# Performance work log

Measured on AMD Instinct MI355X. Metric: run time of the kernel, lower is better.

The kernel has to match this reference:

```python
import jax, jax.numpy as jnp
import numpy as np

COMMITMENT_BETA = 0.25


def setup_inputs() -> dict:
    key = jax.random.key(0)
    k1, k2 = jax.random.split(key)
    B, D, H, W = 32, 256, 32, 32
    NUM_CODES = 1024
    z = jax.random.normal(k1, (B, D, H, W), dtype=jnp.float32)
    codebook = jax.random.normal(k2, (NUM_CODES, D), dtype=jnp.float32)
    return {"z": z, "codebook": codebook}


def reference(z, codebook):
    # z: [B, D, H, W], codebook: [K, D]
    B, D, H, W = z.shape
    z_flat = jnp.transpose(z, (0, 2, 3, 1)).reshape(-1, D)  # [N, D]
    # squared euclidean distances: ||z||^2 - 2 z.W^T + ||W||^2  -> [N, K]
    d = (
        jnp.sum(z_flat * z_flat, axis=1, keepdims=True)
        - 2.0 * (z_flat @ codebook.T)
        + jnp.sum(codebook * codebook, axis=1)[None, :]
    )
    indices = jnp.argmin(d, axis=1)  # [N]
    z_q_flat = codebook[indices]  # [N, D] gather
    # commitment loss: mse(z_flat, stop_grad(z_q_flat))
    diff = z_flat - jax.lax.stop_gradient(z_q_flat)
    commitment_loss = jnp.mean(diff * diff)
    # straight-through estimator
    z_q_flat = z_flat + jax.lax.stop_gradient(z_q_flat - z_flat)
    z_q = jnp.transpose(z_q_flat.reshape(B, H, W, D), (0, 3, 1, 2))
    indices = indices.reshape(B, H, W)
    return z_q, indices, COMMITMENT_BETA * commitment_loss
```

## Files before the change

### kernel.cpp

```cpp
#include <hip/hip_runtime.h>
#include <hip/hip_bf16.h>
#include <hip/hip_fp16.h>

#define DD  256
#define HWD 1024
#define NN  32768
#define KK  1024
#define ZQ_SIZE (NN*DD)
#define IDX_OFF ZQ_SIZE
#define LOSS_OFF (ZQ_SIZE + NN)

#define CBH_OFF    0
#define CNORM_OFF  (KK*DD*2)
#define ZSQ_OFF    (CNORM_OFF + KK*4)
#define ROWREC_OFF (ZSQ_OFF + 4096)

#define TH_REFINE 0.2f
#define LOSS_SCALE (0.25f / (float)ZQ_SIZE)

typedef __attribute__((ext_vector_type(8))) _Float16 h16x8;
typedef __attribute__((ext_vector_type(4))) float f32x4;

__device__ __forceinline__ void gload16(const void* g, void* l) {
    __builtin_amdgcn_global_load_lds(
        (const __attribute__((address_space(1))) void*)g,
        (__attribute__((address_space(3))) void*)l, 16, 0, 0);
}
__device__ __forceinline__ short f16bits(float x) {
    _Float16 h = (_Float16)x;
    return *reinterpret_cast<short*>(&h);
}
__device__ __forceinline__ void ins3(float v, float k, float& u1, float& e1,
                                     float& u2, float& e2, float& u3, float& e3) {
    bool l1 = v < u1, l2 = v < u2, l3 = v < u3;
    u3 = l2 ? u2 : (l3 ? v : u3);  e3 = l2 ? e2 : (l3 ? k : e3);
    u2 = l1 ? u1 : (l2 ? v : u2);  e2 = l1 ? e1 : (l2 ? k : e2);
    u1 = l1 ? v : u1;              e1 = l1 ? k : e1;
}

__global__ __launch_bounds__(256)
void vq_prep_kernel(const float* __restrict__ cb, unsigned char* __restrict__ scratch) {
    _Float16* cbh = (_Float16*)(scratch + CBH_OFF);
    float* cn = (float*)(scratch + CNORM_OFF);
    int t = threadIdx.x;
    int row = blockIdx.x * 16 + (t >> 4);
    int dq  = t & 15;
    const float* rp = cb + (size_t)row * DD + dq * 16;
    float nrm = 0.f;
    __attribute__((aligned(16))) _Float16 h[16];
#pragma unroll
    for (int i = 0; i < 4; ++i) {
        float4 v = *(const float4*)(rp + i * 4);
        float xs[4] = {v.x, v.y, v.z, v.w};
#pragma unroll
        for (int j = 0; j < 4; ++j) {
            float x = xs[j];
            h[i * 4 + j] = (_Float16)x;
            nrm = fmaf(x, x, nrm);
        }
    }
    *(uint4*)&cbh[(size_t)row * DD + dq * 16]     = *(uint4*)&h[0];
    *(uint4*)&cbh[(size_t)row * DD + dq * 16 + 8] = *(uint4*)&h[8];
#pragma unroll
    for (int m = 1; m < 16; m <<= 1) nrm += __shfl_xor(nrm, m, 64);
    if (dq == 0) cn[row] = nrm;
}

__global__ __launch_bounds__(256) __attribute__((amdgpu_waves_per_eu(3, 3)))
void vq_mfma_argmin_kernel(const float* __restrict__ z, unsigned char* __restrict__ scratch) {
    const unsigned char* cbh_b = scratch + CBH_OFF;
    const float* cn_g = (const float*)(scratch + CNORM_OFF);
    float* zsqp = (float*)(scratch + ZSQ_OFF);
    float* rowrec = (float*)(scratch + ROWREC_OFF);

    __shared__ __attribute__((aligned(16))) short bufs[3 * 8192];
    __shared__ float cn_l[512];
    __shared__ float zred[4];
    __shared__ float2 ep[2][64][3];

    const int t    = threadIdx.x;
    const int w    = t >> 6;
    const int lane = t & 63;
    const int ln15 = lane & 15;
    const int lh   = lane >> 4;
    const int g    = w >> 1;
    const int kq   = w & 1;

    const int bid = blockIdx.x;
    const int kh  = bid & 1;
    const int rt  = bid >> 1;
    const int n0  = rt * 64;
    const int b   = n0 >> 10;
    const int hw0 = n0 & 1023;

    const int ksub  = lane >> 5;
    const int chunk = lane & 31;

    const int klr   = kq * 16 + ln15;
    const int rbase = klr * 256;
    const int rxor  = (klr & 7) << 3;

    {
        float2 c = *(const float2*)(cn_g + kh * 512 + t * 2);
        *(float2*)&cn_l[t * 2] = c;
    }

    {
        short* zlds = bufs;
        const int zd = t >> 4;
        const int zq = t & 15;
        const float* zb = z + (size_t)b * DD * HWD + hw0 + zq * 4;
        float zsq = 0.f;
#pragma unroll
        for (int p = 0; p < 16; ++p) {
            int d = p * 16 + zd;
            float4 v = *(const float4*)(zb + (size_t)d * HWD);
            zsq = fmaf(v.x, v.x, zsq); zsq = fmaf(v.y, v.y, zsq);
            zsq = fmaf(v.z, v.z, zsq); zsq = fmaf(v.w, v.w, zsq);
            float xs[4] = {v.x, v.y, v.z, v.w};
#pragma unroll
            for (int i = 0; i < 4; ++i) {
                int row = zq * 4 + i;
                zlds[row * 256 + (d ^ ((row & 15) << 3))] = f16bits(xs[i]);
            }
        }
#pragma unroll
        for (int m = 1; m < 64; m <<= 1) zsq += __shfl_xor(zsq, m, 64);
        if (lane == 0) zred[w] = zsq;
    }
    __syncthreads();

    h16x8 ah[2][8];
#pragma unroll
    for (int nf = 0; nf < 2; ++nf)
#pragma unroll
        for (int ds = 0; ds < 8; ++ds) {
            int row = g * 32 + nf * 16 + ln15;
            int d0  = ds * 32 + lh * 8;
            ah[nf][ds] = *(const h16x8*)&bufs[row * 256 + (d0 ^ ((row & 15) << 3))];
        }
    if (kh == 0 && t == 0) zsqp[rt] = (zred[0] + zred[1]) + (zred[2] + zred[3]);
    __syncthreads();

    auto STAGE = [&](int tt) {
        short* dstb = &bufs[(tt % 3) * 8192];
#pragma unroll
        for (int si = 0; si < 4; ++si) {
            int s  = w * 4 + si;
            int kl = s * 2 + ksub;
            const unsigned char* src = cbh_b
                + (size_t)(kh * 512 + tt * 32 + kl) * 512 + ((chunk ^ (kl & 7)) << 4);
            gload16(src, &dstb[s * 512]);
        }
    };

    float v1[8], k1f[8], v2[8], k2f[8];
#pragma unroll
    for (int s = 0; s < 8; ++s) { v1[s] = 3e38f; v2[s] = 3e38f; k1f[s] = 0.f; k2f[s] = 0.f; }

    auto COMPUTE = [&](int kt) {
        const short* cbt = &bufs[(kt % 3) * 8192];
        const float cnv = cn_l[kt * 32 + klr];
        const float kgf = (float)(kh * 512 + kt * 32 + klr);
        f32x4 c0 = {0.f,0.f,0.f,0.f}, c1 = c0, c2 = c0, c3 = c0;
#pragma unroll
        for (int ds = 0; ds < 8; ds += 2) {
            const int ib0 = rbase + (((ds + 0) * 32 + lh * 8) ^ rxor);
            const int ib1 = rbase + (((ds + 1) * 32 + lh * 8) ^ rxor);
            h16x8 b0 = *(const h16x8*)&cbt[ib0];
            h16x8 b1 = *(const h16x8*)&cbt[ib1];
            c0 = __builtin_amdgcn_mfma_f32_16x16x32_f16(ah[0][ds + 0], b0, c0, 0, 0, 0);
            c2 = __builtin_amdgcn_mfma_f32_16x16x32_f16(ah[1][ds + 0], b0, c2, 0, 0, 0);
            c1 = __builtin_amdgcn_mfma_f32_16x16x32_f16(ah[0][ds + 1], b1, c1, 0, 0, 0);
            c3 = __builtin_amdgcn_mfma_f32_16x16x32_f16(ah[1][ds + 1], b1, c3, 0, 0, 0);
        }
        f32x4 s0 = c0 + c1, s1 = c2 + c3;
#pragma unroll
        for (int s = 0; s < 8; ++s) {
            float a = (s < 4) ? s0[s] : s1[s - 4];
            float dist = fmaf(-2.f, a, cnv);
            bool b1c = dist < v1[s];
            bool b2c = dist < v2[s];
            v2[s]  = b1c ? v1[s]  : (b2c ? dist : v2[s]);
            k2f[s] = b1c ? k1f[s] : (b2c ? kgf  : k2f[s]);
            v1[s]  = b1c ? dist : v1[s];
            k1f[s] = b1c ? kgf  : k1f[s];
        }
    };

    STAGE(0); STAGE(1);

    for (int kt = 0; kt < 14; ++kt) {
        asm volatile("s_waitcnt vmcnt(4)" ::: "memory");
        __builtin_amdgcn_sched_barrier(0);
        __builtin_amdgcn_s_barrier();
        __builtin_amdgcn_sched_barrier(0);
        STAGE(kt + 2);
        COMPUTE(kt);
    }
    asm volatile("s_waitcnt vmcnt(4)" ::: "memory");
    __builtin_amdgcn_sched_barrier(0);
    __builtin_amdgcn_s_barrier();
    __builtin_amdgcn_sched_barrier(0);
    COMPUTE(14);
    asm volatile("s_waitcnt vmcnt(0)" ::: "memory");
    __builtin_amdgcn_sched_barrier(0);
    __builtin_amdgcn_s_barrier();
    __builtin_amdgcn_sched_barrier(0);
    COMPUTE(15);

    float u3[8], e3[8];
#pragma unroll
    for (int s = 0; s < 8; ++s) { u3[s] = 3e38f; e3[s] = 0.f; }
#pragma unroll
    for (int m = 1; m < 16; m <<= 1) {
#pragma unroll
        for (int s = 0; s < 8; ++s) {
            float o1 = __shfl_xor(v1[s],  m, 64);
            float p1 = __shfl_xor(k1f[s], m, 64);
            float o2 = __shfl_xor(v2[s],  m, 64);
            float p2 = __shfl_xor(k2f[s], m, 64);
            float o3 = __shfl_xor(u3[s],  m, 64);
            float p3 = __shfl_xor(e3[s],  m, 64);
            ins3(o1, p1, v1[s], k1f[s], v2[s], k2f[s], u3[s], e3[s]);
            ins3(o2, p2, v1[s], k1f[s], v2[s], k2f[s], u3[s], e3[s]);
            ins3(o3, p3, v1[s], k1f[s], v2[s], k2f[s], u3[s], e3[s]);
        }
    }
    __syncthreads();
    if (ln15 == 0) {
#pragma unroll
        for (int s = 0; s < 8; ++s) {
            int nf = s >> 2, r = s & 3;
            int row = g * 32 + nf * 16 + lh * 4 + r;
            ep[kq][row][0] = make_float2(v1[s], k1f[s]);
            ep[kq][row][1] = make_float2(v2[s], k2f[s]);
            ep[kq][row][2] = make_float2(u3[s], e3[s]);
        }
    }
    __syncthreads();
    if (t < 64) {
        float a1 = 3e38f, b1 = 0.f, a2 = 3e38f, b2 = 0.f, a3 = 3e38f, b3 = 0.f;
#pragma unroll
        for (int q = 0; q < 2; ++q)
#pragma unroll
            for (int e = 0; e < 3; ++e) {
                float2 x = ep[q][t][e];
                ins3(x.x, x.y, a1, b1, a2, b2, a3, b3);
            }
        size_t base = ((size_t)kh * NN + n0 + t) * 8;
        float4 ra; ra.x = a1; ra.y = b1; ra.z = a2; ra.w = b2;
        float4 rb; rb.x = a3; rb.y = b3; rb.z = 0.f; rb.w = 0.f;
        *(float4*)&rowrec[base]     = ra;
        *(float4*)&rowrec[base + 4] = rb;
    }
}

__global__ __launch_bounds__(256)
void vq_refine_kernel(const float* __restrict__ z, const float* __restrict__ cb,
                      const unsigned char* __restrict__ scratch, float* __restrict__ idx_out,
                      float* __restrict__ lossp) {
    const float* rowrec = (const float*)(scratch + ROWREC_OFF);
    const float* cn_g = (const float*)(scratch + CNORM_OFF);
    const float* zsqp = (const float*)(scratch + ZSQ_OFF);
    int n = blockIdx.x * 256 + threadIdx.x;
    int lane = threadIdx.x & 63;

    float u1 = 3e38f, u2 = 3e38f, u3 = 3e38f, e1 = 0.f, e2 = 0.f, e3 = 0.f;
#pragma unroll
    for (int h = 0; h < 2; ++h) {
        size_t base = ((size_t)h * NN + n) * 8;
        float4 ra = *(const float4*)&rowrec[base];
        float4 rb = *(const float4*)&rowrec[base + 4];
        ins3(ra.x, ra.y, u1, e1, u2, e2, u3, e3);
        ins3(ra.z, ra.w, u1, e1, u2, e2, u3, e3);
        ins3(rb.x, rb.y, u1, e1, u2, e2, u3, e3);
    }

    bool flag = (u2 - u1) <= TH_REFINE;
    float lp = 0.f;
    if (!flag) { idx_out[n] = e1; lp = u1; }

    unsigned long long mask = __ballot(flag);
    while (mask) {
        int li = __ffsll(mask) - 1;
        mask &= mask - 1;
        int nn  = __shfl(n, li);
        int kk1 = (int)__shfl(e1, li);
        int kk2 = (int)__shfl(e2, li);
        int kk3 = (int)__shfl(e3, li);
        int bb = nn >> 10, hw = nn & 1023;
        const float* zp  = z  + (size_t)bb * DD * HWD + hw;
        const float* c1p = cb + (size_t)kk1 * DD;
        const float* c2p = cb + (size_t)kk2 * DD;
        const float* c3p = cb + (size_t)kk3 * DD;
        float s1 = 0.f, s2 = 0.f, s3 = 0.f;
#pragma unroll
        for (int j = 0; j < 4; ++j) {
            int d = lane + 64 * j;
            float zv = zp[(size_t)d * HWD];
            s1 = fmaf(zv, c1p[d], s1);
            s2 = fmaf(zv, c2p[d], s2);
            s3 = fmaf(zv, c3p[d], s3);
        }
#pragma unroll
        for (int m = 32; m >= 1; m >>= 1) {
            s1 += __shfl_xor(s1, m, 64);
            s2 += __shfl_xor(s2, m, 64);
            s3 += __shfl_xor(s3, m, 64);
        }
        float d1 = cn_g[kk1] - 2.f * s1;
        float d2 = cn_g[kk2] - 2.f * s2;
        float d3 = cn_g[kk3] - 2.f * s3;
        float dch = d1; int kch = kk1;
        if (d2 < dch || (d2 == dch && kk2 < kch)) { dch = d2; kch = kk2; }
        if (d3 < dch || (d3 == dch && kk3 < kch)) { dch = d3; kch = kk3; }
        if (lane == 0) { idx_out[nn] = (float)kch; lp += dch; }
    }

    if (blockIdx.x == 0) {
        const float2 zv = *(const float2*)&zsqp[threadIdx.x * 2];
        lp += zv.x + zv.y;
    }
#pragma unroll
    for (int m = 32; m >= 1; m >>= 1) lp += __shfl_xor(lp, m, 64);
    __shared__ float bl[4];
    if (lane == 0) bl[threadIdx.x >> 6] = lp;
    __syncthreads();
    if (threadIdx.x == 0)
        atomicAdd(lossp, (bl[0] + bl[1] + bl[2] + bl[3]) * LOSS_SCALE);
}

__global__ __launch_bounds__(256)
void vq_gather_kernel(const float* __restrict__ cb, float* __restrict__ out) {
    const float* idxf = out + IDX_OFF;
    __shared__ float crow[64][257];
    __shared__ int kidx[64];
    int t = threadIdx.x;
    int w = t >> 6, lane = t & 63;
    int n0 = blockIdx.x * 64;
    int b = n0 >> 10, hw0 = n0 & 1023;
    if (t < 64) kidx[t] = (int)idxf[n0 + t];
    __syncthreads();
    for (int i = 0; i < 16; ++i) {
        int r = w * 16 + i;
        int k = kidx[r];
        float4 v = *(const float4*)(cb + (size_t)k * DD + lane * 4);
        crow[r][lane * 4 + 0] = v.x; crow[r][lane * 4 + 1] = v.y;
        crow[r][lane * 4 + 2] = v.z; crow[r][lane * 4 + 3] = v.w;
    }
    __syncthreads();
    const int zph = t >> 6, hwl = t & 63;
#pragma unroll 4
    for (int dd = 0; dd < 64; ++dd) {
        int d = dd * 4 + zph;
        size_t o = (size_t)b * (DD * HWD) + (size_t)d * HWD + hw0 + hwl;
        out[o] = crow[hwl][d];
    }
}

extern "C" void kernel_launch(void* const* d_in, const int* in_sizes, int n_in,
                              void* d_out, int out_size, void* d_ws, size_t ws_size,
                              hipStream_t stream) {
    const float* z  = (const float*)d_in[0];
    const float* cb = (const float*)d_in[1];
    float* out = (float*)d_out;
    unsigned char* scratch = (unsigned char*)d_out;

    hipMemsetAsync((void*)(out + LOSS_OFF), 0, sizeof(float), stream);

    vq_prep_kernel<<<64, 256, 0, stream>>>(cb, scratch);
    vq_mfma_argmin_kernel<<<1024, 256, 0, stream>>>(z, scratch);
    vq_refine_kernel<<<128, 256, 0, stream>>>(z, cb, scratch, out + IDX_OFF, out + LOSS_OFF);
    vq_gather_kernel<<<512, 256, 0, stream>>>(cb, out);
}
```

Before: 82.80 us.

## Split z fp16 conversion into prep kernel and double rows per argmin block

Moves the z transpose, fp16 conversion and norm computation into a separate prep kernel that writes row-major fp16 z to scratch. The argmin kernel now handles 128 rows per block (four 16-row fragments per wave), so each codebook tile staged into LDS is reused across twice as many rows. The codebook pipeline also deepens from three to four buffers. The trade-offs are an extra launch and a scratch round-trip for z, more registers per wave (occupancy hint lowered to 2), and half as many argmin blocks.

```diff
diff --git a/kernel.cpp b/kernel.cpp
--- a/kernel.cpp
+++ b/kernel.cpp
@@ -14,6 +14,7 @@
 #define CNORM_OFF  (KK*DD*2)
 #define ZSQ_OFF    (CNORM_OFF + KK*4)
 #define ROWREC_OFF (ZSQ_OFF + 4096)
+#define Z16_OFF    (4*1024*1024)
 
 #define TH_REFINE 0.2f
 #define LOSS_SCALE (0.25f / (float)ZQ_SIZE)
@@ -66,118 +67,122 @@
     if (dq == 0) cn[row] = nrm;
 }
 
-__global__ __launch_bounds__(256) __attribute__((amdgpu_waves_per_eu(3, 3)))
-void vq_mfma_argmin_kernel(const float* __restrict__ z, unsigned char* __restrict__ scratch) {
+__global__ __launch_bounds__(256)
+void vq_prepz_kernel(const float* __restrict__ z, unsigned char* __restrict__ scratch) {
+    short* z16 = (short*)(scratch + Z16_OFF);
+    float* zsqp = (float*)(scratch + ZSQ_OFF);
+    __shared__ short zl[64 * 256];
+    __shared__ float zred[4];
+    const int t = threadIdx.x, w = t >> 6, lane = t & 63;
+    const int n0 = blockIdx.x * 64;
+    const int b = n0 >> 10, hw0 = n0 & 1023;
+    const int zd = t >> 4;
+    const int zq = t & 15;
+    const float* zb = z + (size_t)b * DD * HWD + hw0 + zq * 4;
+    float zsq = 0.f;
+#pragma unroll
+    for (int p = 0; p < 16; ++p) {
+        int d = p * 16 + zd;
+        float4 v = *(const float4*)(zb + (size_t)d * HWD);
+        zsq = fmaf(v.x, v.x, zsq); zsq = fmaf(v.y, v.y, zsq);
+        zsq = fmaf(v.z, v.z, zsq); zsq = fmaf(v.w, v.w, zsq);
+        float xs[4] = {v.x, v.y, v.z, v.w};
+#pragma unroll
+        for (int i = 0; i < 4; ++i) {
+            int row = zq * 4 + i;
+            zl[row * 256 + (d ^ ((row & 7) << 3))] = f16bits(xs[i]);
+        }
+    }
+#pragma unroll
+    for (int m = 1; m < 64; m <<= 1) zsq += __shfl_xor(zsq, m, 64);
+    if (lane == 0) zred[w] = zsq;
+    __syncthreads();
+    if (t == 0) zsqp[blockIdx.x] = (zred[0] + zred[1]) + (zred[2] + zred[3]);
+#pragma unroll
+    for (int i = 0; i < 8; ++i) {
+        int c = i * 256 + t;
+        int row = c >> 5, ch = c & 31;
+        uint4 v = *(uint4*)&zl[row * 256 + ((ch * 8) ^ ((row & 7) << 3))];
+        *(uint4*)&z16[(size_t)(n0 + row) * 256 + ch * 8] = v;
+    }
+}
+
+__global__ __launch_bounds__(256) __attribute__((amdgpu_waves_per_eu(2, 2)))
+void vq_mfma_argmin_kernel(unsigned char* __restrict__ scratch) {
     const unsigned char* cbh_b = scratch + CBH_OFF;
     const float* cn_g = (const float*)(scratch + CNORM_OFF);
-    float* zsqp = (float*)(scratch + ZSQ_OFF);
+    const short* z16 = (const short*)(scratch + Z16_OFF);
     float* rowrec = (float*)(scratch + ROWREC_OFF);
 
-    __shared__ __attribute__((aligned(16))) short bufs[3 * 8192];
+    __shared__ __attribute__((aligned(16))) short bufs[4 * 8192];
     __shared__ float cn_l[512];
-    __shared__ float zred[4];
-    __shared__ float2 ep[2][64][3];
+    __shared__ float2 ep[2][128][3];
 
     const int t    = threadIdx.x;
     const int w    = t >> 6;
     const int lane = t & 63;
     const int ln15 = lane & 15;
     const int lh   = lane >> 4;
-    const int g    = w >> 1;
-    const int kq   = w & 1;
+    const int rg   = w >> 1;
+    const int kh   = w & 1;
 
     const int bid = blockIdx.x;
-    const int kh  = bid & 1;
+    const int kq  = bid & 1;
     const int rt  = bid >> 1;
-    const int n0  = rt * 64;
-    const int b   = n0 >> 10;
-    const int hw0 = n0 & 1023;
+    const int n0  = rt * 128;
 
     const int ksub  = lane >> 5;
     const int chunk = lane & 31;
 
-    const int klr   = kq * 16 + ln15;
+    const int klr   = kh * 16 + ln15;
     const int rbase = klr * 256;
     const int rxor  = (klr & 7) << 3;
 
-    {
-        float2 c = *(const float2*)(cn_g + kh * 512 + t * 2);
-        *(float2*)&cn_l[t * 2] = c;
-    }
-
-    {
-        short* zlds = bufs;
-        const int zd = t >> 4;
-        const int zq = t & 15;
-        const float* zb = z + (size_t)b * DD * HWD + hw0 + zq * 4;
-        float zsq = 0.f;
-#pragma unroll
-        for (int p = 0; p < 16; ++p) {
-            int d = p * 16 + zd;
-            float4 v = *(const float4*)(zb + (size_t)d * HWD);
-            zsq = fmaf(v.x, v.x, zsq); zsq = fmaf(v.y, v.y, zsq);
-            zsq = fmaf(v.z, v.z, zsq); zsq = fmaf(v.w, v.w, zsq);
-            float xs[4] = {v.x, v.y, v.z, v.w};
-#pragma unroll
-            for (int i = 0; i < 4; ++i) {
-                int row = zq * 4 + i;
-                zlds[row * 256 + (d ^ ((row & 15) << 3))] = f16bits(xs[i]);
-            }
-        }
-#pragma unroll
-        for (int m = 1; m < 64; m <<= 1) zsq += __shfl_xor(zsq, m, 64);
-        if (lane == 0) zred[w] = zsq;
-    }
-    __syncthreads();
-
-    h16x8 ah[2][8];
-#pragma unroll
-    for (int nf = 0; nf < 2; ++nf)
-#pragma unroll
-        for (int ds = 0; ds < 8; ++ds) {
-            int row = g * 32 + nf * 16 + ln15;
-            int d0  = ds * 32 + lh * 8;
-            ah[nf][ds] = *(const h16x8*)&bufs[row * 256 + (d0 ^ ((row & 15) << 3))];
-        }
-    if (kh == 0 && t == 0) zsqp[rt] = (zred[0] + zred[1]) + (zred[2] + zred[3]);
+    *(float2*)&cn_l[t * 2] = *(const float2*)(cn_g + kq * 512 + t * 2);
+
+    h16x8 ah[4][8];
+#pragma unroll
+    for (int nf = 0; nf < 4; ++nf) {
+        const size_t rowb = (size_t)(n0 + rg * 64 + nf * 16 + ln15) * 256;
+#pragma unroll
+        for (int ds = 0; ds < 8; ++ds)
+            ah[nf][ds] = *(const h16x8*)&z16[rowb + ds * 32 + lh * 8];
+    }
     __syncthreads();
 
     auto STAGE = [&](int tt) {
-        short* dstb = &bufs[(tt % 3) * 8192];
+        short* dstb = &bufs[(tt & 3) * 8192];
 #pragma unroll
         for (int si = 0; si < 4; ++si) {
             int s  = w * 4 + si;
             int kl = s * 2 + ksub;
             const unsigned char* src = cbh_b
-                + (size_t)(kh * 512 + tt * 32 + kl) * 512 + ((chunk ^ (kl & 7)) << 4);
+                + (size_t)(kq * 512 + tt * 32 + kl) * 512 + ((chunk ^ (kl & 7)) << 4);
             gload16(src, &dstb[s * 512]);
         }
     };
 
-    float v1[8], k1f[8], v2[8], k2f[8];
-#pragma unroll
-    for (int s = 0; s < 8; ++s) { v1[s] = 3e38f; v2[s] = 3e38f; k1f[s] = 0.f; k2f[s] = 0.f; }
+    float v1[16], k1f[16], v2[16], k2f[16];
+#pragma unroll
+    for (int s = 0; s < 16; ++s) { v1[s] = 3e38f; v2[s] = 3e38f; k1f[s] = 0.f; k2f[s] = 0.f; }
 
     auto COMPUTE = [&](int kt) {
-        const short* cbt = &bufs[(kt % 3) * 8192];
+        const short* cbt = &bufs[(kt & 3) * 8192];
         const float cnv = cn_l[kt * 32 + klr];
-        const float kgf = (float)(kh * 512 + kt * 32 + klr);
-        f32x4 c0 = {0.f,0.f,0.f,0.f}, c1 = c0, c2 = c0, c3 = c0;
-#pragma unroll
-        for (int ds = 0; ds < 8; ds += 2) {
-            const int ib0 = rbase + (((ds + 0) * 32 + lh * 8) ^ rxor);
-            const int ib1 = rbase + (((ds + 1) * 32 + lh * 8) ^ rxor);
-            h16x8 b0 = *(const h16x8*)&cbt[ib0];
-            h16x8 b1 = *(const h16x8*)&cbt[ib1];
-            c0 = __builtin_amdgcn_mfma_f32_16x16x32_f16(ah[0][ds + 0], b0, c0, 0, 0, 0);
-            c2 = __builtin_amdgcn_mfma_f32_16x16x32_f16(ah[1][ds + 0], b0, c2, 0, 0, 0);
-            c1 = __builtin_amdgcn_mfma_f32_16x16x32_f16(ah[0][ds + 1], b1, c1, 0, 0, 0);
-            c3 = __builtin_amdgcn_mfma_f32_16x16x32_f16(ah[1][ds + 1], b1, c3, 0, 0, 0);
-        }
-        f32x4 s0 = c0 + c1, s1 = c2 + c3;
-#pragma unroll
-        for (int s = 0; s < 8; ++s) {
-            float a = (s < 4) ? s0[s] : s1[s - 4];
+        const float kgf = (float)(kq * 512 + kt * 32 + klr);
+        f32x4 a0 = {0.f,0.f,0.f,0.f}, a1 = a0, a2 = a0, a3 = a0;
+#pragma unroll
+        for (int ds = 0; ds < 8; ++ds) {
+            const int ib = rbase + ((ds * 32 + lh * 8) ^ rxor);
+            h16x8 bh = *(const h16x8*)&cbt[ib];
+            a0 = __builtin_amdgcn_mfma_f32_16x16x32_f16(ah[0][ds], bh, a0, 0, 0, 0);
+            a1 = __builtin_amdgcn_mfma_f32_16x16x32_f16(ah[1][ds], bh, a1, 0, 0, 0);
+            a2 = __builtin_amdgcn_mfma_f32_16x16x32_f16(ah[2][ds], bh, a2, 0, 0, 0);
+            a3 = __builtin_amdgcn_mfma_f32_16x16x32_f16(ah[3][ds], bh, a3, 0, 0, 0);
+        }
+#pragma unroll
+        for (int s = 0; s < 16; ++s) {
+            float a = (s < 4) ? a0[s] : (s < 8) ? a1[s - 4] : (s < 12) ? a2[s - 8] : a3[s - 12];
             float dist = fmaf(-2.f, a, cnv);
             bool b1c = dist < v1[s];
             bool b2c = dist < v2[s];
@@ -188,16 +193,21 @@
         }
     };
 
-    STAGE(0); STAGE(1);
-
-    for (int kt = 0; kt < 14; ++kt) {
-        asm volatile("s_waitcnt vmcnt(4)" ::: "memory");
+    STAGE(0); STAGE(1); STAGE(2);
+
+    for (int kt = 0; kt < 13; ++kt) {
+        asm volatile("s_waitcnt vmcnt(8)" ::: "memory");
         __builtin_amdgcn_sched_barrier(0);
         __builtin_amdgcn_s_barrier();
         __builtin_amdgcn_sched_barrier(0);
-        STAGE(kt + 2);
+        STAGE(kt + 3);
         COMPUTE(kt);
     }
+    asm volatile("s_waitcnt vmcnt(8)" ::: "memory");
+    __builtin_amdgcn_sched_barrier(0);
+    __builtin_amdgcn_s_barrier();
+    __builtin_amdgcn_sched_barrier(0);
+    COMPUTE(13);
     asm volatile("s_waitcnt vmcnt(4)" ::: "memory");
     __builtin_amdgcn_sched_barrier(0);
     __builtin_amdgcn_s_barrier();
@@ -209,13 +219,13 @@
     __builtin_amdgcn_sched_barrier(0);
     COMPUTE(15);
 
-    float u3[8], e3[8];
-#pragma unroll
-    for (int s = 0; s < 8; ++s) { u3[s] = 3e38f; e3[s] = 0.f; }
+    float u3[16], e3[16];
+#pragma unroll
+    for (int s = 0; s < 16; ++s) { u3[s] = 3e38f; e3[s] = 0.f; }
 #pragma unroll
     for (int m = 1; m < 16; m <<= 1) {
 #pragma unroll
-        for (int s = 0; s < 8; ++s) {
+        for (int s = 0; s < 16; ++s) {
             float o1 = __shfl_xor(v1[s],  m, 64);
             float p1 = __shfl_xor(k1f[s], m, 64);
             float o2 = __shfl_xor(v2[s],  m, 64);
@@ -227,19 +237,18 @@
             ins3(o3, p3, v1[s], k1f[s], v2[s], k2f[s], u3[s], e3[s]);
         }
     }
-    __syncthreads();
     if (ln15 == 0) {
 #pragma unroll
-        for (int s = 0; s < 8; ++s) {
+        for (int s = 0; s < 16; ++s) {
             int nf = s >> 2, r = s & 3;
-            int row = g * 32 + nf * 16 + lh * 4 + r;
-            ep[kq][row][0] = make_float2(v1[s], k1f[s]);
-            ep[kq][row][1] = make_float2(v2[s], k2f[s]);
-            ep[kq][row][2] = make_float2(u3[s], e3[s]);
-        }
-    }
-    __syncthreads();
-    if (t < 64) {
+            int rl = rg * 64 + nf * 16 + lh * 4 + r;
+            ep[kh][rl][0] = make_float2(v1[s], k1f[s]);
+            ep[kh][rl][1] = make_float2(v2[s], k2f[s]);
+            ep[kh][rl][2] = make_float2(u3[s], e3[s]);
+        }
+    }
+    __syncthreads();
+    if (t < 128) {
         float a1 = 3e38f, b1 = 0.f, a2 = 3e38f, b2 = 0.f, a3 = 3e38f, b3 = 0.f;
 #pragma unroll
         for (int q = 0; q < 2; ++q)
@@ -248,7 +257,7 @@
                 float2 x = ep[q][t][e];
                 ins3(x.x, x.y, a1, b1, a2, b2, a3, b3);
             }
-        size_t base = ((size_t)kh * NN + n0 + t) * 8;
+        size_t base = ((size_t)kq * NN + n0 + t) * 8;
         float4 ra; ra.x = a1; ra.y = b1; ra.z = a2; ra.w = b2;
         float4 rb; rb.x = a3; rb.y = b3; rb.z = 0.f; rb.w = 0.f;
         *(float4*)&rowrec[base]     = ra;
@@ -370,7 +379,8 @@
     hipMemsetAsync((void*)(out + LOSS_OFF), 0, sizeof(float), stream);
 
     vq_prep_kernel<<<64, 256, 0, stream>>>(cb, scratch);
-    vq_mfma_argmin_kernel<<<1024, 256, 0, stream>>>(z, scratch);
+    vq_prepz_kernel<<<512, 256, 0, stream>>>(z, scratch);
+    vq_mfma_argmin_kernel<<<512, 256, 0, stream>>>(scratch);
     vq_refine_kernel<<<128, 256, 0, stream>>>(z, cb, scratch, out + IDX_OFF, out + LOSS_OFF);
     vq_gather_kernel<<<512, 256, 0, stream>>>(cb, out);
 }
```

Measured after the change: 83.42 us. Within noise of the previous version (+0.7%).
